# Kernel tuning notes

Measured on AMD Instinct MI355X. Metric: run time of the kernel, lower is better.

## Reference

```python
import jax, jax.numpy as jnp
import numpy as np

DILATION = 64
KERNEL = 2

def setup_inputs() -> dict:
    key = jax.random.key(0)
    k1, k2 = jax.random.split(key)
    x = jax.random.normal(k1, (16, 64, 16384), dtype=jnp.float32)
    w = jax.random.normal(k2, (64, 64, KERNEL), dtype=jnp.float32) * 0.1
    return {"x": x, "w": w}

def _causal_dilated_conv(x, w):
    # left-pad by dilation*(kernel_size-1) for causality
    pad = DILATION * (KERNEL - 1)
    xp = jnp.pad(x, ((0, 0), (0, 0), (pad, 0)))
    return jax.lax.conv_general_dilated(
        xp, w,
        window_strides=(1,),
        padding='VALID',
        rhs_dilation=(DILATION,),
        dimension_numbers=('NCH', 'OIH', 'NCH'))

def reference(x, w):
    y = _causal_dilated_conv(x, w)          # [B, C_out, T]
    return jnp.tanh(y) * jax.nn.sigmoid(y)  # fused gate
```

## Files before the change

kernel.cpp:

```cpp
#include <hip/hip_runtime.h>


#define B_ 16
#define C_ 64
#define T_ 16384
#define RING 128

typedef __attribute__((ext_vector_type(8))) short short8;
typedef __attribute__((ext_vector_type(4))) float f32x4;

union Frag { short8 s; unsigned u[4]; };

__device__ __forceinline__ unsigned bf16_rne(float f) {
    unsigned u = __float_as_uint(f);
    return (u + 0x7fffu + ((u >> 16) & 1u)) >> 16;
}

__device__ __forceinline__ unsigned pack_rne(float a, float b) {
    unsigned ua = __float_as_uint(a), ub = __float_as_uint(b);
    unsigned ra = ua + 0x7fffu + ((ua >> 16) & 1u);
    unsigned rb = ub + 0x7fffu + ((ub >> 16) & 1u);
    return (ra >> 16) | (rb & 0xffff0000u);
}

#define EPILOGUE(A, KK)                                                     \
    _Pragma("unroll")                                                       \
    for (int s = 0; s < 4; ++s) {                                           \
        float4 o4;                                                          \
        _Pragma("unroll")                                                   \
        for (int r = 0; r < 4; ++r) {                                       \
            float y = (A)[s][r];                                            \
            y = fminf(fmaxf(y, -20.f), 20.f);                               \
            float e   = __expf(-y);                                         \
            float e2  = e * e;                                              \
            float num = 1.f - e2;                                           \
            float den = (1.f + e) * (1.f + e2);                             \
            ((float*)&o4)[r] = num * __builtin_amdgcn_rcpf(den);            \
        }                                                                   \
        *(float4*)(ob + (KK) * 64 + 16 * s + 4 * q) = o4;                   \
    }

__global__ __launch_bounds__(256, 4) void conv_gate_ring4(
    const float* __restrict__ x,
    const float* __restrict__ w,
    float* __restrict__ out)
{
    __shared__ unsigned short xs[RING * 64];

    const int tid = threadIdx.x;
    const int bid = blockIdx.x;
    const int wg  = (bid & 7) * 128 + (bid >> 3);
    const int b   = wg >> 6;
    const int seg = wg & 63;
    const int t0  = seg << 8;
    const float* xb = x + (size_t)b * C_ * T_;

    float pv[4][8];
    #pragma unroll
    for (int it = 0; it < 4; ++it) {
        const int task = it * 256 + tid;
        const int rr   = task & 127;
        const int c8   = task >> 7;
        const int g    = t0 - 64 + rr;
        if (g >= 0) {
            const float* xp = xb + (size_t)(8 * c8) * T_ + g;
            #pragma unroll
            for (int i = 0; i < 8; ++i) pv[it][i] = xp[(size_t)i * T_];
        } else {
            #pragma unroll
            for (int i = 0; i < 8; ++i) pv[it][i] = 0.f;
        }
    }

    const int lane = tid & 63;
    const int wid  = tid >> 6;
    const int m    = lane & 15;
    const int q    = lane >> 4;
    const int co   = wid * 16 + m;

    Frag wh[2][2], wl[2][2];
    #pragma unroll
    for (int h = 0; h < 2; ++h) {
        const float* wp = w + co * 128 + h * 64 + q * 16;
        float f[16];
        #pragma unroll
        for (int v4 = 0; v4 < 4; ++v4) {
            float4 t4 = *(const float4*)(wp + 4 * v4);
            f[4*v4+0] = t4.x; f[4*v4+1] = t4.y; f[4*v4+2] = t4.z; f[4*v4+3] = t4.w;
        }
        #pragma unroll
        for (int p = 0; p < 2; ++p) {
            #pragma unroll
            for (int d = 0; d < 4; ++d) {
                float e0 = f[2*(2*d)   + p];
                float e1 = f[2*(2*d+1) + p];
                unsigned h0 = bf16_rne(e0), h1 = bf16_rne(e1);
                float r0 = e0 - __uint_as_float(h0 << 16);
                float r1 = e1 - __uint_as_float(h1 << 16);
                wh[p][h].u[d] = h0 | (h1 << 16);
                wl[p][h].u[d] = bf16_rne(r0) | (bf16_rne(r1) << 16);
            }
        }
    }

    #pragma unroll
    for (int it = 0; it < 4; ++it) {
        const int task = it * 256 + tid;
        const int rr   = task & 127;
        const int c8   = task >> 7;
        unsigned p0 = pack_rne(pv[it][0], pv[it][1]);
        unsigned p1 = pack_rne(pv[it][2], pv[it][3]);
        unsigned p2 = pack_rne(pv[it][4], pv[it][5]);
        unsigned p3 = pack_rne(pv[it][6], pv[it][7]);
        const int slot = (rr + 64) & 127;
        const int so   = slot * 64 + ((c8 ^ (rr & 7)) * 8);
        *(uint4*)(&xs[so]) = make_uint4(p0, p1, p2, p3);
    }

    const int n   = m;
    const int swb = n & 7;
    float* ob = out + ((size_t)b * C_ + wid * 16 + m) * T_ + t0;

    f32x4 acc2[2][4];

    __syncthreads();

    #pragma unroll
    for (int k = 0; k < 4; ++k) {
        float v[2][8];
        if (k < 3) {
            #pragma unroll
            for (int it = 0; it < 2; ++it) {
                const int task = it * 256 + tid;
                const int rr = task & 63, c8 = task >> 6;
                const float* xp = xb + (size_t)(8 * c8) * T_ + (t0 + 64 * (k + 1) + rr);
                #pragma unroll
                for (int i = 0; i < 8; ++i) v[it][i] = xp[(size_t)i * T_];
            }
        }

        if (k > 0) { EPILOGUE(acc2[(k & 1) ^ 1], k - 1); }

        f32x4* acc = acc2[k & 1];
        #pragma unroll
        for (int s = 0; s < 4; ++s) acc[s] = (f32x4){0.f, 0.f, 0.f, 0.f};
        const int kb = ((k & 1) ^ 1) << 6;
        #pragma unroll
        for (int u = 0; u < 8; ++u) {
            const int rbase = ((kb + 16 * u + n) & 127) * 64;
            Frag f0, f1;
            f0.s = *(const short8*)(&xs[rbase + ((q ^ swb) * 8)]);
            f1.s = *(const short8*)(&xs[rbase + (((4 + q) ^ swb) * 8)]);
            if (u < 4) {
                acc[u] = __builtin_amdgcn_mfma_f32_16x16x32_bf16(f0.s, wh[0][0].s, acc[u], 0, 0, 0);
                acc[u] = __builtin_amdgcn_mfma_f32_16x16x32_bf16(f0.s, wl[0][0].s, acc[u], 0, 0, 0);
                acc[u] = __builtin_amdgcn_mfma_f32_16x16x32_bf16(f1.s, wh[0][1].s, acc[u], 0, 0, 0);
                acc[u] = __builtin_amdgcn_mfma_f32_16x16x32_bf16(f1.s, wl[0][1].s, acc[u], 0, 0, 0);
            } else {
                const int s2 = u - 4;
                acc[s2] = __builtin_amdgcn_mfma_f32_16x16x32_bf16(f0.s, wh[1][0].s, acc[s2], 0, 0, 0);
                acc[s2] = __builtin_amdgcn_mfma_f32_16x16x32_bf16(f0.s, wl[1][0].s, acc[s2], 0, 0, 0);
                acc[s2] = __builtin_amdgcn_mfma_f32_16x16x32_bf16(f1.s, wh[1][1].s, acc[s2], 0, 0, 0);
                acc[s2] = __builtin_amdgcn_mfma_f32_16x16x32_bf16(f1.s, wl[1][1].s, acc[s2], 0, 0, 0);
            }
        }

        if (k < 3) {
            __syncthreads();

            #pragma unroll
            for (int it = 0; it < 2; ++it) {
                const int task = it * 256 + tid;
                const int rr = task & 63, c8 = task >> 6;
                unsigned p0 = pack_rne(v[it][0], v[it][1]);
                unsigned p1 = pack_rne(v[it][2], v[it][3]);
                unsigned p2 = pack_rne(v[it][4], v[it][5]);
                unsigned p3 = pack_rne(v[it][6], v[it][7]);
                const int slot = (64 * (k + 1) + rr) & 127;
                const int so   = slot * 64 + ((c8 ^ (rr & 7)) * 8);
                *(uint4*)(&xs[so]) = make_uint4(p0, p1, p2, p3);
            }

            __syncthreads();
        }
    }

    EPILOGUE(acc2[1], 3);
}

extern "C" void kernel_launch(void* const* d_in, const int* in_sizes, int n_in,
                              void* d_out, int out_size, void* d_ws, size_t ws_size,
                              hipStream_t stream) {
    const float* x = (const float*)d_in[0];
    const float* w = (const float*)d_in[1];
    float* out = (float*)d_out;
    conv_gate_ring4<<<dim3(1024), dim3(256), 0, stream>>>(x, w, out);
}
```

Before: 125.7 us.

## Use triple-buffered LDS windows with register double-buffered prefetch and simpler gate math

Replaces the 128-row LDS ring with three 64-row windows. Global loads are issued two windows ahead into double-buffered registers, and the LDS store for the next window happens before the MFMA loop, which removes one barrier per iteration. The gate epilogue is rewritten algebraically as (1-u)/(1+u^2) with a single clamp, which cuts ALU work. The cost is more LDS (24KB vs 16KB) and more registers, which may pressure the 4-block occupancy target.

```diff
diff --git a/kernel.cpp b/kernel.cpp
--- a/kernel.cpp
+++ b/kernel.cpp
@@ -4,7 +4,6 @@
 #define B_ 16
 #define C_ 64
 #define T_ 16384
-#define RING 128
 
 typedef __attribute__((ext_vector_type(8))) short short8;
 typedef __attribute__((ext_vector_type(4))) float f32x4;
@@ -29,23 +28,20 @@
         float4 o4;                                                          \
         _Pragma("unroll")                                                   \
         for (int r = 0; r < 4; ++r) {                                       \
-            float y = (A)[s][r];                                            \
-            y = fminf(fmaxf(y, -20.f), 20.f);                               \
-            float e   = __expf(-y);                                         \
-            float e2  = e * e;                                              \
-            float num = 1.f - e2;                                           \
-            float den = (1.f + e) * (1.f + e2);                             \
-            ((float*)&o4)[r] = num * __builtin_amdgcn_rcpf(den);            \
+            float y = fmaxf((A)[s][r], -30.f);                              \
+            float u = __expf(-y);                                           \
+            ((float*)&o4)[r] = (1.f - u) *                                  \
+                __builtin_amdgcn_rcpf(__builtin_fmaf(u, u, 1.f));           \
         }                                                                   \
         *(float4*)(ob + (KK) * 64 + 16 * s + 4 * q) = o4;                   \
     }
 
-__global__ __launch_bounds__(256, 4) void conv_gate_ring4(
+__global__ __launch_bounds__(256, 4) void conv_gate_pipe(
     const float* __restrict__ x,
     const float* __restrict__ w,
     float* __restrict__ out)
 {
-    __shared__ unsigned short xs[RING * 64];
+    __shared__ unsigned short xs[3 * 64 * 64];
 
     const int tid = threadIdx.x;
     const int bid = blockIdx.x;
@@ -70,6 +66,16 @@
             #pragma unroll
             for (int i = 0; i < 8; ++i) pv[it][i] = 0.f;
         }
+    }
+
+    float vbuf[2][2][8];
+    #pragma unroll
+    for (int it = 0; it < 2; ++it) {
+        const int task = it * 256 + tid;
+        const int rr = task & 63, c8 = task >> 6;
+        const float* xp = xb + (size_t)(8 * c8) * T_ + (t0 + 64 + rr);
+        #pragma unroll
+        for (int i = 0; i < 8; ++i) vbuf[0][it][i] = xp[(size_t)i * T_];
     }
 
     const int lane = tid & 63;
@@ -112,8 +118,7 @@
         unsigned p1 = pack_rne(pv[it][2], pv[it][3]);
         unsigned p2 = pack_rne(pv[it][4], pv[it][5]);
         unsigned p3 = pack_rne(pv[it][6], pv[it][7]);
-        const int slot = (rr + 64) & 127;
-        const int so   = slot * 64 + ((c8 ^ (rr & 7)) * 8);
+        const int so = (rr >> 6) * 4096 + (rr & 63) * 64 + ((c8 ^ (rr & 7)) * 8);
         *(uint4*)(&xs[so]) = make_uint4(p0, p1, p2, p3);
     }
 
@@ -127,27 +132,40 @@
 
     #pragma unroll
     for (int k = 0; k < 4; ++k) {
-        float v[2][8];
-        if (k < 3) {
+        if (k <= 1) {
             #pragma unroll
             for (int it = 0; it < 2; ++it) {
                 const int task = it * 256 + tid;
                 const int rr = task & 63, c8 = task >> 6;
-                const float* xp = xb + (size_t)(8 * c8) * T_ + (t0 + 64 * (k + 1) + rr);
+                const float* xp = xb + (size_t)(8 * c8) * T_ + (t0 + 64 * (k + 2) + rr);
                 #pragma unroll
-                for (int i = 0; i < 8; ++i) v[it][i] = xp[(size_t)i * T_];
+                for (int i = 0; i < 8; ++i) vbuf[(k + 1) & 1][it][i] = xp[(size_t)i * T_];
             }
         }
 
-        if (k > 0) { EPILOGUE(acc2[(k & 1) ^ 1], k - 1); }
+        if (k >= 1) { EPILOGUE(acc2[(k & 1) ^ 1], k - 1); }
+
+        if (k <= 2) {
+            #pragma unroll
+            for (int it = 0; it < 2; ++it) {
+                const int task = it * 256 + tid;
+                const int rr = task & 63, c8 = task >> 6;
+                unsigned p0 = pack_rne(vbuf[k & 1][it][0], vbuf[k & 1][it][1]);
+                unsigned p1 = pack_rne(vbuf[k & 1][it][2], vbuf[k & 1][it][3]);
+                unsigned p2 = pack_rne(vbuf[k & 1][it][4], vbuf[k & 1][it][5]);
+                unsigned p3 = pack_rne(vbuf[k & 1][it][6], vbuf[k & 1][it][7]);
+                const int so = ((k + 2) % 3) * 4096 + rr * 64 + ((c8 ^ (rr & 7)) * 8);
+                *(uint4*)(&xs[so]) = make_uint4(p0, p1, p2, p3);
+            }
+        }
 
         f32x4* acc = acc2[k & 1];
         #pragma unroll
         for (int s = 0; s < 4; ++s) acc[s] = (f32x4){0.f, 0.f, 0.f, 0.f};
-        const int kb = ((k & 1) ^ 1) << 6;
         #pragma unroll
         for (int u = 0; u < 8; ++u) {
-            const int rbase = ((kb + 16 * u + n) & 127) * 64;
+            const int wnd   = k + (u >> 2);
+            const int rbase = (wnd % 3) * 4096 + (16 * (u & 3) + n) * 64;
             Frag f0, f1;
             f0.s = *(const short8*)(&xs[rbase + ((q ^ swb) * 8)]);
             f1.s = *(const short8*)(&xs[rbase + (((4 + q) ^ swb) * 8)]);
@@ -165,24 +183,7 @@
             }
         }
 
-        if (k < 3) {
-            __syncthreads();
-
-            #pragma unroll
-            for (int it = 0; it < 2; ++it) {
-                const int task = it * 256 + tid;
-                const int rr = task & 63, c8 = task >> 6;
-                unsigned p0 = pack_rne(v[it][0], v[it][1]);
-                unsigned p1 = pack_rne(v[it][2], v[it][3]);
-                unsigned p2 = pack_rne(v[it][4], v[it][5]);
-                unsigned p3 = pack_rne(v[it][6], v[it][7]);
-                const int slot = (64 * (k + 1) + rr) & 127;
-                const int so   = slot * 64 + ((c8 ^ (rr & 7)) * 8);
-                *(uint4*)(&xs[so]) = make_uint4(p0, p1, p2, p3);
-            }
-
-            __syncthreads();
-        }
+        if (k < 3) __syncthreads();
     }
 
     EPILOGUE(acc2[1], 3);
@@ -194,5 +195,5 @@
     const float* x = (const float*)d_in[0];
     const float* w = (const float*)d_in[1];
     float* out = (float*)d_out;
-    conv_gate_ring4<<<dim3(1024), dim3(256), 0, stream>>>(x, w, out);
+    conv_gate_pipe<<<dim3(1024), dim3(256), 0, stream>>>(x, w, out);
 }
```

Measured after the change: 126.8 us. About the same (+0.8%).
